# Optimization experiments

Measured on AMD Instinct MI355X. Metric: run time of the kernel, lower is better.

## Reference

```python
import jax, jax.numpy as jnp
import numpy as np

LN_EPS = 1e-5
NEG_SLOPE = 0.01  # torch LeakyReLU default


def layernorm(x, w, b):
    m = jnp.mean(x, axis=-1, keepdims=True)
    v = jnp.mean((x - m) ** 2, axis=-1, keepdims=True)
    return (x - m) * jax.lax.rsqrt(v + LN_EPS) * w + b


def setup_inputs() -> dict:
    key = jax.random.key(0)
    ks = jax.random.split(key, 12)
    B, T, C, E = 16, 1024, 768, 2
    d = C
    s = 0.02
    inp = {
        "x": jax.random.normal(ks[0], (B, T, C), jnp.float32),
        "ln1_w": jnp.ones((C,), jnp.float32),
        "ln1_b": jnp.zeros((C,), jnp.float32),
        "wqkv": jax.random.normal(ks[1], (C, 3 * C), jnp.float32) * s,
        "bqkv": jnp.zeros((3 * C,), jnp.float32),
        "wproj": jax.random.normal(ks[2], (C, C), jnp.float32) * s,
        "bproj": jnp.zeros((C,), jnp.float32),
        "ln2_w": jnp.ones((C,), jnp.float32),
        "ln2_b": jnp.zeros((C,), jnp.float32),
        "wg": jax.random.normal(ks[3], (C, E), jnp.float32) * s,
        # Experts module uses torch.randn (std 1); we scale down for numerics
        "w1": jax.random.normal(ks[4], (E, d, 4 * d), jnp.float32) * s,
        "w2": jax.random.normal(ks[5], (E, 4 * d, 4 * d), jnp.float32) * s,
        "w3": jax.random.normal(ks[6], (E, 4 * d, d), jnp.float32) * s,
        "n_head": 12,
    }
    return inp


def block_forward(x, ln1_w, ln1_b, wqkv, bqkv, wproj, bproj,
                  ln2_w, ln2_b, wg, w1, w2, w3, n_head):
    B, T, C = x.shape
    H = n_head
    hd = C // H
    E = wg.shape[-1]

    # ---- causal self-attention + residual ----
    h = layernorm(x, ln1_w, ln1_b)
    qkv = h @ wqkv + bqkv                      # [B,T,3C]
    q, k, v = jnp.split(qkv, 3, axis=-1)
    q = q.reshape(B, T, H, hd).transpose(0, 2, 1, 3)  # bhtd
    k = k.reshape(B, T, H, hd).transpose(0, 2, 1, 3)
    v = v.reshape(B, T, H, hd).transpose(0, 2, 1, 3)
    scores = jnp.einsum('bhqd,bhkd->bhqk', q, k) / jnp.sqrt(jnp.float32(hd))
    causal = jnp.tril(jnp.ones((T, T), bool))
    scores = jnp.where(causal, scores, jnp.finfo(scores.dtype).min)
    attn = jax.nn.softmax(scores, axis=-1)
    y = jnp.einsum('bhqk,bhkd->bhqd', attn, v)
    y = y.transpose(0, 2, 1, 3).reshape(B, T, C)
    x = x + (y @ wproj + bproj)

    # ---- MoE (top-2 gating, capacity dispatch) + residual ----
    h2 = layernorm(x, ln2_w, ln2_b)
    capacity = (T * 2) // E                    # capacity_factor = 1.0, top-2
    raw_gates = jax.nn.softmax(h2 @ wg, axis=-1)   # [B,T,E]

    idx1 = jnp.argmax(raw_gates, axis=-1)
    mask1 = jax.nn.one_hot(idx1, E, dtype=raw_gates.dtype)
    gate1 = jnp.sum(raw_gates * mask1, axis=-1)    # [B,T]
    gates2 = raw_gates * (1.0 - mask1)
    idx2 = jnp.argmax(gates2, axis=-1)
    mask2 = jax.nn.one_hot(idx2, E, dtype=raw_gates.dtype)
    gate2 = jnp.sum(raw_gates * mask2, axis=-1)
    denom = gate1 + gate2 + 1e-9
    gate1, gate2 = gate1 / denom, gate2 / denom

    # aux load-balancing loss (before capacity truncation)
    density = jnp.mean(mask1, axis=1)              # [B,E]
    density_proxy = jnp.mean(raw_gates, axis=1)    # [B,E]
    aux_loss = jnp.mean(density * density_proxy) * (E * E)

    # positions within each expert buffer (exclusive cumsum over tokens)
    pos1 = jnp.cumsum(mask1, axis=1) - mask1       # [B,T,E]
    mask1 = mask1 * (pos1 < capacity)
    mask1_count = jnp.sum(mask1, axis=1, keepdims=True)
    pos2 = (jnp.cumsum(mask2, axis=1) - mask2) + mask1_count
    mask2 = mask2 * (pos2 < capacity)

    oh1 = jax.nn.one_hot(pos1.astype(jnp.int32), capacity, dtype=raw_gates.dtype)
    oh2 = jax.nn.one_hot(pos2.astype(jnp.int32), capacity, dtype=raw_gates.dtype)
    combine = (gate1[..., None] * mask1)[..., None] * oh1 \
            + (gate2[..., None] * mask2)[..., None] * oh2   # [B,T,E,C]
    dispatch = (combine > 0).astype(h2.dtype)

    # dispatch -> per-expert batches
    expert_in = jnp.einsum('bnd,bnec->ebcd', h2, dispatch)   # [E,B,Cap,d]
    Bc = B * capacity
    ei = expert_in.reshape(E, Bc, C)
    lrelu = lambda z: jnp.where(z >= 0, z, NEG_SLOPE * z)
    hh = lrelu(jnp.einsum('end,edh->enh', ei, w1))
    hh = lrelu(jnp.einsum('end,edh->enh', hh, w2))
    eo = jnp.einsum('end,edh->enh', hh, w3).reshape(E, B, capacity, C)
    moe_out = jnp.einsum('ebcd,bnec->bnd', eo, combine)

    x = x + moe_out
    return x, aux_loss


def reference(x, ln1_w, ln1_b, wqkv, bqkv, wproj, bproj,
              ln2_w, ln2_b, wg, w1, w2, w3, n_head):
    return block_forward(x, ln1_w, ln1_b, wqkv, bqkv, wproj, bproj,
                         ln2_w, ln2_b, wg, w1, w2, w3, n_head)
```

## Files before the change

### kernel.cpp

```cpp
#include <hip/hip_runtime.h>
#include <cstdint>
#include <cstddef>

constexpr int B_  = 16;
constexpr int T_  = 1024;
constexpr int C_  = 768;
constexpr int H_  = 12;
constexpr int HD_ = 64;
constexpr int BT_ = B_ * T_;
constexpr int C3_ = 3 * C_;
constexpr int QK2_ = 2 * C_;
constexpr int FF_ = 4 * C_;
constexpr int MCH_ = 8192;

typedef __bf16 bf16x8 __attribute__((ext_vector_type(8)));
typedef float  floatx4 __attribute__((ext_vector_type(4)));
typedef unsigned short u16x8 __attribute__((ext_vector_type(8)));

__device__ inline float bf2f(unsigned short u) {
  union { unsigned int i; float f; } x; x.i = ((unsigned int)u) << 16; return x.f;
}
__device__ inline unsigned short f2bf(float f) {
  union { float f; unsigned int i; } x; x.f = f;
  unsigned int u = x.i;
  u += 0x7fffu + ((u >> 16) & 1u);
  return (unsigned short)(u >> 16);
}

#define GLOAD_LDS16(gp, lp)                                              \
  __builtin_amdgcn_global_load_lds(                                      \
      (__attribute__((address_space(1))) void*)(gp),                     \
      (__attribute__((address_space(3))) void*)(lp), 16, 0, 0)

__launch_bounds__(256)
__global__ void ln_kernel(const float* __restrict__ x, const float* __restrict__ w,
                          const float* __restrict__ b, unsigned short* __restrict__ out) {
  int row = blockIdx.x;
  int tid = threadIdx.x;
  const float* xr = x + (size_t)row * C_;
  float v0 = xr[tid], v1 = xr[tid + 256], v2 = xr[tid + 512];
  float s  = v0 + v1 + v2;
  float ss = v0 * v0 + v1 * v1 + v2 * v2;
#pragma unroll
  for (int off = 32; off > 0; off >>= 1) {
    s  += __shfl_down(s, off, 64);
    ss += __shfl_down(ss, off, 64);
  }
  __shared__ float red[8];
  int wid = tid >> 6;
  if ((tid & 63) == 0) { red[wid] = s; red[4 + wid] = ss; }
  __syncthreads();
  float st  = red[0] + red[1] + red[2] + red[3];
  float sst = red[4] + red[5] + red[6] + red[7];
  float mean = st * (1.0f / C_);
  float var  = sst * (1.0f / C_) - mean * mean;
  float rstd = rsqrtf(var + 1e-5f);
  unsigned short* orow = out + (size_t)row * C_;
  orow[tid]       = f2bf((v0 - mean) * rstd * w[tid]       + b[tid]);
  orow[tid + 256] = f2bf((v1 - mean) * rstd * w[tid + 256] + b[tid + 256]);
  orow[tid + 512] = f2bf((v2 - mean) * rstd * w[tid + 512] + b[tid + 512]);
}

__launch_bounds__(256)
__global__ void convT(const float* __restrict__ in, unsigned short* __restrict__ out,
                      int K, int N) {
  __shared__ float t[32][33];
  int n0 = blockIdx.x * 32, k0 = blockIdx.y * 32;
  int tx = threadIdx.x & 31, ty = threadIdx.x >> 5;
#pragma unroll
  for (int r = 0; r < 32; r += 8)
    t[r + ty][tx] = in[(size_t)(k0 + r + ty) * N + n0 + tx];
  __syncthreads();
#pragma unroll
  for (int r = 0; r < 32; r += 8)
    out[(size_t)(n0 + r + ty) * K + k0 + tx] = f2bf(t[tx][r + ty]);
}

template <int ACT, bool BIAS, bool RES, bool COMBINE, bool OUTBF16, bool VSPLIT = false>
__launch_bounds__(256)
__global__ void gemm_bf16(const unsigned short* __restrict__ A,
                          const unsigned short* __restrict__ Bt,
                          const float* __restrict__ bias,
                          const float* __restrict__ Rres,
                          const float* __restrict__ gates2, int eidx,
                          void* __restrict__ Cout,
                          unsigned short* __restrict__ vtout,
                          int M, int N, int K) {
  __shared__ __attribute__((aligned(16))) unsigned short Als[8192];
  __shared__ __attribute__((aligned(16))) unsigned short Bls[8192];
  const int tid  = threadIdx.x;
  const int wave = tid >> 6, lane = tid & 63;
  const int wr = wave >> 1, wc = wave & 1;
  const int m0 = blockIdx.y * 128, n0 = blockIdx.x * 128;

  const int srow = wave * 32 + (lane >> 3);
  const int skg  = (lane & 7) ^ ((lane >> 3) & 7);
  const unsigned short* Ap = A  + (size_t)(m0 + srow) * K + skg * 8;
  const unsigned short* Bp = Bt + (size_t)(n0 + srow) * K + skg * 8;
  unsigned short* AlsW = Als + wave * 2048;
  unsigned short* BlsW = Bls + wave * 2048;

  floatx4 acc[4][4];
#pragma unroll
  for (int i = 0; i < 4; ++i)
#pragma unroll
    for (int j = 0; j < 4; ++j) acc[i][j] = floatx4{0.f, 0.f, 0.f, 0.f};

  const int q  = lane >> 4;
  const int ml = lane & 15;
  const int rsw = ml & 7;

  for (int k0 = 0; k0 < K; k0 += 64) {
    __syncthreads();
#pragma unroll
    for (int i = 0; i < 4; ++i) {
      GLOAD_LDS16(Ap + (size_t)(i * 8) * K + k0, AlsW + i * 512);
      GLOAD_LDS16(Bp + (size_t)(i * 8) * K + k0, BlsW + i * 512);
    }
    __syncthreads();
#pragma unroll
    for (int ks = 0; ks < 2; ++ks) {
      const int p = (ks * 4 + q) ^ rsw;
      bf16x8 af[4], bfg[4];
#pragma unroll
      for (int i = 0; i < 4; ++i) {
        int ar = wr * 64 + i * 16 + ml;
        af[i]  = *(const bf16x8*)&Als[(ar * 8 + p) * 8];
        int br = wc * 64 + i * 16 + ml;
        bfg[i] = *(const bf16x8*)&Bls[(br * 8 + p) * 8];
      }
#pragma unroll
      for (int i = 0; i < 4; ++i)
#pragma unroll
        for (int j = 0; j < 4; ++j)
          acc[i][j] = __builtin_amdgcn_mfma_f32_16x16x32_bf16(af[i], bfg[j], acc[i][j], 0, 0, 0);
    }
  }

  const int rbase = q * 4;
#pragma unroll
  for (int i = 0; i < 4; ++i) {
    int row = m0 + wr * 64 + i * 16 + rbase;
#pragma unroll
    for (int j = 0; j < 4; ++j) {
      int col = n0 + wc * 64 + j * 16 + ml;
      float bcol = BIAS ? bias[col] : 0.f;
#pragma unroll
      for (int r = 0; r < 4; ++r) {
        float v = acc[i][j][r];
        if (BIAS) v += bcol;
        if (ACT == 1) v = (v >= 0.f) ? v : 0.01f * v;
        if (RES) v += Rres[(size_t)(row + r) * N + col];
        if (COMBINE) {
          float g = gates2[2 * (row + r) + eidx];
          float* op = (float*)Cout + (size_t)(row + r) * N + col;
          *op += g * v;
        } else if (VSPLIT) {
          if (col < QK2_) {
            ((unsigned short*)Cout)[(size_t)(row + r) * QK2_ + col] = f2bf(v);
          } else {
            vtout[(size_t)(col - QK2_) * BT_ + row + r] = f2bf(v);
          }
        } else if (OUTBF16) {
          ((unsigned short*)Cout)[(size_t)(row + r) * N + col] = f2bf(v);
        } else {
          ((float*)Cout)[(size_t)(row + r) * N + col] = v;
        }
      }
    }
  }
}

#define GB256_BAR()   asm volatile("s_barrier" ::: "memory")
#define GB256_LGKM0() asm volatile("s_waitcnt lgkmcnt(0)" ::: "memory")

template <int ACT, bool BIAS>
__launch_bounds__(512, 2)
__global__ void gemm256(const unsigned short* __restrict__ A,
                        const unsigned short* __restrict__ Bt,
                        const float* __restrict__ bias,
                        unsigned short* __restrict__ Cout,
                        int M, int N, int K) {
  __shared__ __attribute__((aligned(16))) unsigned short L[65536];
  const int tid = threadIdx.x;
  const int w = tid >> 6, l = tid & 63;
  const int wr = w >> 2, wc = w & 3;
  const int ml = l & 15, q = l >> 4;
  const int m0 = blockIdx.y * 256, n0 = blockIdx.x * 256;

  const int srow = l >> 2;
  const int sg   = ((l & 3) ^ ((l >> 3) & 3)) * 8;
  const unsigned short* Ast = A  + (size_t)(m0 + srow) * K + sg;
  const unsigned short* Bst = Bt + (size_t)(n0 + srow) * K + sg;
  const int ldsw = w * 1024;

#define STG(cb, mat, ks, srcp, kk)                                           \
  do {                                                                       \
    const unsigned short* _s = (srcp) + (size_t)(w * 32) * K + (kk) + (ks) * 32; \
    unsigned short* _d = L + (cb) * 32768 + (mat) * 16384 + (ks) * 8192 + ldsw;  \
    GLOAD_LDS16(_s, _d);                                                     \
    GLOAD_LDS16(_s + (size_t)16 * K, _d + 512);                              \
  } while (0)

  const int dphys = (q ^ ((ml >> 1) & 3)) * 8;
  const int aoff = (wr * 128 + ml) * 32 + dphys;
  const int boff = (wc * 64 + ml) * 32 + dphys;

  floatx4 acc[8][4];
#pragma unroll
  for (int m = 0; m < 8; ++m)
#pragma unroll
    for (int n = 0; n < 4; ++n) acc[m][n] = floatx4{0.f, 0.f, 0.f, 0.f};

  const int NT = K >> 6;

  STG(0, 0, 0, Ast, 0);  STG(0, 1, 0, Bst, 0);
  STG(0, 0, 1, Ast, 0);  STG(0, 1, 1, Bst, 0);
  STG(1, 0, 0, Ast, 64); STG(1, 1, 0, Bst, 64);
  asm volatile("s_waitcnt vmcnt(0)" ::: "memory");
  GB256_BAR();

  for (int j = 0; j < NT; ++j) {
    const int c = j & 1, nx = c ^ 1;
    const int kk1 = (j + 1) << 6, kk2 = (j + 2) << 6;
    const bool st1 = (j + 1 < NT), st2 = (j + 2 < NT);
    bf16x8 bA[4], bB[4];

#define LOAD_A(KS, MH)                                                       \
  _Pragma("unroll")                                                          \
  for (int mq = 0; mq < 4; ++mq)                                             \
    bA[mq] = *(const bf16x8*)&L[c * 32768 + (KS) * 8192 + aoff + ((MH) * 4 + mq) * 512];
#define LOAD_B(KS)                                                           \
  _Pragma("unroll")                                                          \
  for (int n = 0; n < 4; ++n)                                                \
    bB[n] = *(const bf16x8*)&L[c * 32768 + 16384 + (KS) * 8192 + boff + n * 512];
#define MFMA16(MH)                                                           \
  __builtin_amdgcn_s_setprio(1);                                             \
  _Pragma("unroll")                                                          \
  for (int mq = 0; mq < 4; ++mq)                                             \
    _Pragma("unroll")                                                        \
    for (int n = 0; n < 4; ++n)                                              \
      acc[(MH) * 4 + mq][n] = __builtin_amdgcn_mfma_f32_16x16x32_bf16(       \
          bA[mq], bB[n], acc[(MH) * 4 + mq][n], 0, 0, 0);                    \
  __builtin_amdgcn_s_setprio(0);

    LOAD_B(0); LOAD_A(0, 0);
    if (st1) STG(nx, 0, 1, Ast, kk1);
    GB256_BAR(); GB256_LGKM0();
    MFMA16(0);
    GB256_BAR();

    LOAD_A(0, 1);
    if (st1) STG(nx, 1, 1, Bst, kk1);
    GB256_BAR(); GB256_LGKM0();
    MFMA16(1);
    GB256_BAR();

    LOAD_B(1); LOAD_A(1, 0);
    if (st2) STG(c, 0, 0, Ast, kk2);
    GB256_BAR(); GB256_LGKM0();
    MFMA16(0);
    GB256_BAR();

    LOAD_A(1, 1);
    if (st2) STG(c, 1, 0, Bst, kk2);
    GB256_BAR(); GB256_LGKM0();
    MFMA16(1);
    if (st2)      asm volatile("s_waitcnt vmcnt(4)" ::: "memory");
    else if (st1) asm volatile("s_waitcnt vmcnt(0)" ::: "memory");
    GB256_BAR();
#undef LOAD_A
#undef LOAD_B
#undef MFMA16
  }

#pragma unroll
  for (int m = 0; m < 8; ++m) {
    const int row = m0 + wr * 128 + m * 16 + q * 4;
#pragma unroll
    for (int n = 0; n < 4; ++n) {
      const int col = n0 + wc * 64 + n * 16 + ml;
      const float bcol = BIAS ? bias[col] : 0.f;
#pragma unroll
      for (int r = 0; r < 4; ++r) {
        float v = acc[m][n][r];
        if (BIAS) v += bcol;
        if (ACT == 1) v = (v >= 0.f) ? v : 0.01f * v;
        Cout[(size_t)(row + r) * N + col] = f2bf(v);
      }
    }
  }
#undef STG
}

__launch_bounds__(256)
__global__ void attn_kernel(const unsigned short* __restrict__ qk,
                            const unsigned short* __restrict__ vT,
                            unsigned short* __restrict__ y) {
  __shared__ __attribute__((aligned(16))) unsigned short Qls[64 * 64];
  __shared__ __attribute__((aligned(16))) unsigned short K2[2][64 * 64];
  __shared__ __attribute__((aligned(16))) unsigned short V2[2][64 * 64];
  __shared__ __attribute__((aligned(16))) unsigned short Pls[4 * 16 * 72];

  const int tid  = threadIdx.x;
  const int wave = tid >> 6, lane = tid & 63;
  const int quad = lane >> 4, n = lane & 15;
  const int q0 = blockIdx.x * 64;
  const int bh = blockIdx.y;
  const int b = bh / H_, h = bh % H_;
  const size_t qbase = (size_t)b * T_ * QK2_ + (size_t)h * HD_;
  const size_t vbase = (size_t)h * HD_ * BT_ + (size_t)b * T_;

  const int r8 = lane >> 3;
  const int g  = (lane & 7) ^ r8;

#pragma unroll
  for (int i = 0; i < 2; ++i) {
    int row = wave * 16 + i * 8 + r8;
    GLOAD_LDS16(qk + qbase + (size_t)(q0 + row) * QK2_ + g * 8,
                Qls + wave * 1024 + i * 512);
  }

#define STAGE_KV(bf, k0)                                                      \
  do {                                                                        \
    _Pragma("unroll")                                                         \
    for (int i = 0; i < 2; ++i) {                                             \
      int row = wave * 16 + i * 8 + r8;                                       \
      GLOAD_LDS16(qk + qbase + (size_t)((k0) + row) * QK2_ + C_ + g * 8,      \
                  K2[bf] + wave * 1024 + i * 512);                            \
      GLOAD_LDS16(vT + vbase + (size_t)row * BT_ + (k0) + g * 8,              \
                  V2[bf] + wave * 1024 + i * 512);                            \
    }                                                                         \
  } while (0)

  STAGE_KV(0, 0);

  floatx4 O[4];
#pragma unroll
  for (int ct = 0; ct < 4; ++ct) O[ct] = floatx4{0.f, 0.f, 0.f, 0.f};
  float mrow[4] = {-1e30f, -1e30f, -1e30f, -1e30f};
  float lrow[4] = {0.f, 0.f, 0.f, 0.f};

  const int nkt = blockIdx.x + 1;
  unsigned short* Pw = Pls + wave * (16 * 72);

  for (int kt = 0; kt < nkt; ++kt) {
    const int cur = kt & 1;
    __syncthreads();
    if (kt + 1 < nkt) STAGE_KV(cur ^ 1, (kt + 1) << 6);

    floatx4 sacc[4];
#pragma unroll
    for (int ct = 0; ct < 4; ++ct) sacc[ct] = floatx4{0.f, 0.f, 0.f, 0.f};
#pragma unroll
    for (int ks = 0; ks < 2; ++ks) {
      const int ga = (ks * 4 + quad) ^ (n & 7);
      bf16x8 aq = *(const bf16x8*)&Qls[((wave * 16 + n) * 8 + ga) * 8];
#pragma unroll
      for (int ct = 0; ct < 4; ++ct) {
        bf16x8 kb = *(const bf16x8*)&K2[cur][((ct * 16 + n) * 8 + ga) * 8];
        sacc[ct] = __builtin_amdgcn_mfma_f32_16x16x32_bf16(aq, kb, sacc[ct], 0, 0, 0);
      }
    }

    float p[4][4];
#pragma unroll
    for (int ct = 0; ct < 4; ++ct)
#pragma unroll
      for (int r = 0; r < 4; ++r) p[ct][r] = sacc[ct][r] * 0.125f;
    if (kt == nkt - 1) {
      const int kgb = (kt << 6) + n, qgb = q0 + wave * 16 + quad * 4;
#pragma unroll
      for (int ct = 0; ct < 4; ++ct)
#pragma unroll
        for (int r = 0; r < 4; ++r)
          if (kgb + ct * 16 > qgb + r) p[ct][r] = -1e30f;
    }
#pragma unroll
    for (int r = 0; r < 4; ++r) {
      float tm = fmaxf(fmaxf(p[0][r], p[1][r]), fmaxf(p[2][r], p[3][r]));
      tm = fmaxf(tm, __shfl_xor(tm, 1, 64));
      tm = fmaxf(tm, __shfl_xor(tm, 2, 64));
      tm = fmaxf(tm, __shfl_xor(tm, 4, 64));
      tm = fmaxf(tm, __shfl_xor(tm, 8, 64));
      float mn = fmaxf(mrow[r], tm);
      float alpha = __expf(mrow[r] - mn);
      mrow[r] = mn;
      float ps = 0.f;
#pragma unroll
      for (int ct = 0; ct < 4; ++ct) {
        float pe = __expf(p[ct][r] - mn);
        p[ct][r] = pe;
        ps += pe;
      }
      ps += __shfl_xor(ps, 1, 64);
      ps += __shfl_xor(ps, 2, 64);
      ps += __shfl_xor(ps, 4, 64);
      ps += __shfl_xor(ps, 8, 64);
      lrow[r] = lrow[r] * alpha + ps;
      O[0][r] *= alpha; O[1][r] *= alpha; O[2][r] *= alpha; O[3][r] *= alpha;
    }

#pragma unroll
    for (int ct = 0; ct < 4; ++ct)
#pragma unroll
      for (int r = 0; r < 4; ++r)
        Pw[(quad * 4 + r) * 72 + ct * 16 + n] = f2bf(p[ct][r]);

#pragma unroll
    for (int ks = 0; ks < 2; ++ks) {
      bf16x8 pa = *(const bf16x8*)&Pw[n * 72 + (ks * 4 + quad) * 8];
      const int gv = (ks * 4 + quad) ^ (n & 7);
#pragma unroll
      for (int ct = 0; ct < 4; ++ct) {
        bf16x8 vb = *(const bf16x8*)&V2[cur][((ct * 16 + n) * 8 + gv) * 8];
        O[ct] = __builtin_amdgcn_mfma_f32_16x16x32_bf16(pa, vb, O[ct], 0, 0, 0);
      }
    }
  }

#pragma unroll
  for (int r = 0; r < 4; ++r) {
    float inv = 1.0f / lrow[r];
    int row = q0 + wave * 16 + quad * 4 + r;
    unsigned short* dst = y + ((size_t)b * T_ + row) * C_ + h * HD_;
#pragma unroll
    for (int ct = 0; ct < 4; ++ct)
      dst[ct * 16 + n] = f2bf(O[ct][r] * inv);
  }
#undef STAGE_KV
}

__launch_bounds__(256)
__global__ void gate_kernel(const unsigned short* __restrict__ h2,
                            const float* __restrict__ wg,
                            float* __restrict__ gates) {
  int wave = threadIdx.x >> 6, lane = threadIdx.x & 63;
  int t = blockIdx.x * 4 + wave;
  const unsigned short* hr = h2 + (size_t)t * C_;
  float a0 = 0.0f, a1 = 0.0f;
#pragma unroll
  for (int i = 0; i < 12; ++i) {
    int d = lane + 64 * i;
    float hv = bf2f(hr[d]);
    a0 += hv * wg[2 * d];
    a1 += hv * wg[2 * d + 1];
  }
#pragma unroll
  for (int off = 32; off > 0; off >>= 1) {
    a0 += __shfl_down(a0, off, 64);
    a1 += __shfl_down(a1, off, 64);
  }
  if (lane == 0) {
    float m  = fmaxf(a0, a1);
    float e0 = __expf(a0 - m), e1 = __expf(a1 - m);
    float invs = 1.0f / (e0 + e1);
    float p0 = e0 * invs, p1 = e1 * invs;
    const float gnorm = 1.0f / (1.0f + 1e-9f);
    gates[2 * t]     = p0 * gnorm;
    gates[2 * t + 1] = p1 * gnorm;
  }
}

__launch_bounds__(1024)
__global__ void moe_stats_kernel(const float* __restrict__ gates,
                                 float* __restrict__ out_aux) {
  int wave = threadIdx.x >> 6, lane = threadIdx.x & 63;
  float c0 = 0.f, sp0 = 0.f, sp1 = 0.f;
#pragma unroll
  for (int j = 0; j < 16; ++j) {
    int t = wave * T_ + lane + 64 * j;
    float p0 = gates[2 * t], p1 = gates[2 * t + 1];
    c0  += (p1 > p0) ? 0.f : 1.f;
    sp0 += p0;
    sp1 += p1;
  }
#pragma unroll
  for (int off = 32; off > 0; off >>= 1) {
    c0  += __shfl_down(c0, off, 64);
    sp0 += __shfl_down(sp0, off, 64);
    sp1 += __shfl_down(sp1, off, 64);
  }
  __shared__ float red[16][3];
  if (lane == 0) { red[wave][0] = c0; red[wave][1] = sp0; red[wave][2] = sp1; }
  __syncthreads();
  if (threadIdx.x == 0) {
    float s = 0.f;
    for (int b = 0; b < B_; ++b) {
      float cc0 = red[b][0];
      float d0 = cc0 * (1.f / T_), d1 = (T_ - cc0) * (1.f / T_);
      float px0 = red[b][1] * (1.f / T_), px1 = red[b][2] * (1.f / T_);
      s += d0 * px0 + d1 * px1;
    }
    out_aux[0] = s * (4.f / 32.f);
  }
}

extern "C" void kernel_launch(void* const* d_in, const int* in_sizes, int n_in,
                              void* d_out, int out_size, void* d_ws, size_t ws_size,
                              hipStream_t stream) {
  const float* x     = (const float*)d_in[0];
  const float* ln1_w = (const float*)d_in[1];
  const float* ln1_b = (const float*)d_in[2];
  const float* wqkv  = (const float*)d_in[3];
  const float* bqkv  = (const float*)d_in[4];
  const float* wproj = (const float*)d_in[5];
  const float* bproj = (const float*)d_in[6];
  const float* ln2_w = (const float*)d_in[7];
  const float* ln2_b = (const float*)d_in[8];
  const float* wg    = (const float*)d_in[9];
  const float* w1    = (const float*)d_in[10];
  const float* w2    = (const float*)d_in[11];
  const float* w3    = (const float*)d_in[12];
  float* out = (float*)d_out;

  unsigned short* wsu   = (unsigned short*)d_ws;
  unsigned short* wqkvT = wsu;
  unsigned short* wprojT= wqkvT + (size_t)C3_ * C_;
  unsigned short* w1T   = wprojT + (size_t)C_ * C_;
  unsigned short* w2T   = w1T + (size_t)2 * FF_ * C_;
  unsigned short* w3T   = w2T + (size_t)2 * FF_ * FF_;
  unsigned short* hb    = w3T + (size_t)2 * C_ * FF_;
  unsigned short* region= hb + (size_t)BT_ * C_;
  unsigned short* qkb   = region;
  unsigned short* vTb   = region + (size_t)BT_ * QK2_;
  unsigned short* yb    = region + (size_t)BT_ * 3 * C_;
  unsigned short* hh1   = region;
  unsigned short* hh2   = region + (size_t)MCH_ * FF_;
  float* gates = (float*)(region + (size_t)BT_ * 4 * C_);

  convT<<<dim3(C3_ / 32, C_ / 32), 256, 0, stream>>>(wqkv, wqkvT, C_, C3_);
  convT<<<dim3(C_ / 32, C_ / 32), 256, 0, stream>>>(wproj, wprojT, C_, C_);
  for (int e = 0; e < 2; ++e) {
    convT<<<dim3(FF_ / 32, C_ / 32), 256, 0, stream>>>(
        w1 + (size_t)e * C_ * FF_, w1T + (size_t)e * FF_ * C_, C_, FF_);
    convT<<<dim3(FF_ / 32, FF_ / 32), 256, 0, stream>>>(
        w2 + (size_t)e * FF_ * FF_, w2T + (size_t)e * FF_ * FF_, FF_, FF_);
    convT<<<dim3(C_ / 32, FF_ / 32), 256, 0, stream>>>(
        w3 + (size_t)e * FF_ * C_, w3T + (size_t)e * C_ * FF_, FF_, C_);
  }

  ln_kernel<<<BT_, 256, 0, stream>>>(x, ln1_w, ln1_b, hb);
  gemm_bf16<0, true, false, false, true, true><<<dim3(C3_ / 128, BT_ / 128), 256, 0, stream>>>(
      hb, wqkvT, bqkv, nullptr, nullptr, 0, qkb, vTb, BT_, C3_, C_);
  attn_kernel<<<dim3(T_ / 64, B_ * H_), 256, 0, stream>>>(qkb, vTb, yb);
  gemm_bf16<0, true, true, false, false><<<dim3(C_ / 128, BT_ / 128), 256, 0, stream>>>(
      yb, wprojT, bproj, x, nullptr, 0, out, nullptr, BT_, C_, C_);

  ln_kernel<<<BT_, 256, 0, stream>>>(out, ln2_w, ln2_b, hb);
  gate_kernel<<<BT_ / 4, 256, 0, stream>>>(hb, wg, gates);
  moe_stats_kernel<<<1, 1024, 0, stream>>>(gates, out + (size_t)BT_ * C_);

  for (int e = 0; e < 2; ++e) {
    for (int c = 0; c < BT_ / MCH_; ++c) {
      const unsigned short* a = hb + (size_t)c * MCH_ * C_;
      gemm_bf16<1, false, false, false, true><<<dim3(FF_ / 128, MCH_ / 128), 256, 0, stream>>>(
          a, w1T + (size_t)e * FF_ * C_, nullptr, nullptr, nullptr, 0, hh1, nullptr, MCH_, FF_, C_);
      gemm256<1, false><<<dim3(FF_ / 256, MCH_ / 256), 512, 0, stream>>>(
          hh1, w2T + (size_t)e * FF_ * FF_, nullptr, hh2, MCH_, FF_, FF_);
      gemm_bf16<0, false, false, true, false><<<dim3(C_ / 128, MCH_ / 128), 256, 0, stream>>>(
          hh2, w3T + (size_t)e * C_ * FF_, nullptr, nullptr,
          gates + (size_t)2 * c * MCH_, e, out + (size_t)c * MCH_ * C_, nullptr, MCH_, C_, FF_);
    }
  }
}
```

Measured before the change: 1.811 ms.

## Double-buffer LDS fragment registers in gemm256 and use it for FFN1

```diff
diff --git a/kernel.cpp b/kernel.cpp
--- a/kernel.cpp
+++ b/kernel.cpp
@@ -171,8 +171,8 @@
   }
 }
 
-#define GB256_BAR()   asm volatile("s_barrier" ::: "memory")
-#define GB256_LGKM0() asm volatile("s_waitcnt lgkmcnt(0)" ::: "memory")
+#define GB256_BAR()  asm volatile("s_barrier" ::: "memory")
+#define SCHEDB0()    __builtin_amdgcn_sched_barrier(0)
 
 template <int ACT, bool BIAS>
 __launch_bounds__(512, 2)
@@ -220,59 +220,73 @@
   asm volatile("s_waitcnt vmcnt(0)" ::: "memory");
   GB256_BAR();
 
-  for (int j = 0; j < NT; ++j) {
-    const int c = j & 1, nx = c ^ 1;
-    const int kk1 = (j + 1) << 6, kk2 = (j + 2) << 6;
-    const bool st1 = (j + 1 < NT), st2 = (j + 2 < NT);
-    bf16x8 bA[4], bB[4];
-
-#define LOAD_A(KS, MH)                                                       \
+  bf16x8 rA0[4], rA1[4], rB0[4], rB1[4];
+#pragma unroll
+  for (int mq = 0; mq < 4; ++mq)
+    rA0[mq] = *(const bf16x8*)&L[aoff + mq * 512];
+#pragma unroll
+  for (int n = 0; n < 4; ++n)
+    rB0[n] = *(const bf16x8*)&L[16384 + boff + n * 512];
+
+#define LDA(dst, CB, KS, MH)                                                 \
   _Pragma("unroll")                                                          \
   for (int mq = 0; mq < 4; ++mq)                                             \
-    bA[mq] = *(const bf16x8*)&L[c * 32768 + (KS) * 8192 + aoff + ((MH) * 4 + mq) * 512];
-#define LOAD_B(KS)                                                           \
+    dst[mq] = *(const bf16x8*)&L[(CB) * 32768 + (KS) * 8192 + aoff + ((MH) * 4 + mq) * 512];
+#define LDB(dst, CB, KS)                                                     \
   _Pragma("unroll")                                                          \
   for (int n = 0; n < 4; ++n)                                                \
-    bB[n] = *(const bf16x8*)&L[c * 32768 + 16384 + (KS) * 8192 + boff + n * 512];
-#define MFMA16(MH)                                                           \
+    dst[n] = *(const bf16x8*)&L[(CB) * 32768 + 16384 + (KS) * 8192 + boff + n * 512];
+#define MFMA16(MH, AR, BR)                                                   \
   __builtin_amdgcn_s_setprio(1);                                             \
   _Pragma("unroll")                                                          \
   for (int mq = 0; mq < 4; ++mq)                                             \
     _Pragma("unroll")                                                        \
     for (int n = 0; n < 4; ++n)                                              \
       acc[(MH) * 4 + mq][n] = __builtin_amdgcn_mfma_f32_16x16x32_bf16(       \
-          bA[mq], bB[n], acc[(MH) * 4 + mq][n], 0, 0, 0);                    \
+          AR[mq], BR[n], acc[(MH) * 4 + mq][n], 0, 0, 0);                    \
   __builtin_amdgcn_s_setprio(0);
 
-    LOAD_B(0); LOAD_A(0, 0);
+  for (int j = 0; j < NT; ++j) {
+    const int c = j & 1, nx = c ^ 1;
+    const int kk1 = (j + 1) << 6, kk2 = (j + 2) << 6;
+    const bool st1 = (j + 1 < NT), st2 = (j + 2 < NT);
+
+    LDA(rA1, c, 0, 1);
     if (st1) STG(nx, 0, 1, Ast, kk1);
-    GB256_BAR(); GB256_LGKM0();
-    MFMA16(0);
+    SCHEDB0();
+    MFMA16(0, rA0, rB0);
     GB256_BAR();
 
-    LOAD_A(0, 1);
+    LDB(rB1, c, 1);
+    LDA(rA0, c, 1, 0);
     if (st1) STG(nx, 1, 1, Bst, kk1);
-    GB256_BAR(); GB256_LGKM0();
-    MFMA16(1);
+    SCHEDB0();
+    MFMA16(1, rA1, rB0);
     GB256_BAR();
 
-    LOAD_B(1); LOAD_A(1, 0);
+    LDA(rA1, c, 1, 1);
     if (st2) STG(c, 0, 0, Ast, kk2);
-    GB256_BAR(); GB256_LGKM0();
-    MFMA16(0);
+    SCHEDB0();
+    MFMA16(0, rA0, rB1);
+    if (st2)      asm volatile("s_waitcnt vmcnt(6)" ::: "memory");
+    else if (st1) asm volatile("s_waitcnt vmcnt(4)" ::: "memory");
+    else          asm volatile("s_waitcnt vmcnt(0)" ::: "memory");
     GB256_BAR();
 
-    LOAD_A(1, 1);
+    if (st1) {
+      LDA(rA0, nx, 0, 0);
+      LDB(rB0, nx, 0);
+    }
     if (st2) STG(c, 1, 0, Bst, kk2);
-    GB256_BAR(); GB256_LGKM0();
-    MFMA16(1);
-    if (st2)      asm volatile("s_waitcnt vmcnt(4)" ::: "memory");
-    else if (st1) asm volatile("s_waitcnt vmcnt(0)" ::: "memory");
+    SCHEDB0();
+    MFMA16(1, rA1, rB1);
+    if (st2) asm volatile("s_waitcnt vmcnt(4)" ::: "memory");
+    else     asm volatile("s_waitcnt vmcnt(0)" ::: "memory");
     GB256_BAR();
-#undef LOAD_A
-#undef LOAD_B
+  }
+#undef LDA
+#undef LDB
 #undef MFMA16
-  }
 
 #pragma unroll
   for (int m = 0; m < 8; ++m) {
@@ -554,8 +568,8 @@
   for (int e = 0; e < 2; ++e) {
     for (int c = 0; c < BT_ / MCH_; ++c) {
       const unsigned short* a = hb + (size_t)c * MCH_ * C_;
-      gemm_bf16<1, false, false, false, true><<<dim3(FF_ / 128, MCH_ / 128), 256, 0, stream>>>(
-          a, w1T + (size_t)e * FF_ * C_, nullptr, nullptr, nullptr, 0, hh1, nullptr, MCH_, FF_, C_);
+      gemm256<1, false><<<dim3(FF_ / 256, MCH_ / 256), 512, 0, stream>>>(
+          a, w1T + (size_t)e * FF_ * C_, nullptr, hh1, MCH_, FF_, C_);
       gemm256<1, false><<<dim3(FF_ / 256, MCH_ / 256), 512, 0, stream>>>(
           hh1, w2T + (size_t)e * FF_ * FF_, nullptr, hh2, MCH_, FF_, FF_);
       gemm_bf16<0, false, false, true, false><<<dim3(C_ / 128, MCH_ / 128), 256, 0, stream>>>(
```

Measured after the change: 1.878 ms. +3.7%, slower.

## Batch both MoE experts into z-dimension grids and merge weight transposes

Applied to the files above, without the earlier changes.

```diff
diff --git a/kernel.cpp b/kernel.cpp
--- a/kernel.cpp
+++ b/kernel.cpp
@@ -61,12 +61,27 @@
   orow[tid + 512] = f2bf((v2 - mean) * rstd * w[tid + 512] + b[tid + 512]);
 }
 
+struct CtJobs {
+  const float* in[8];
+  unsigned short* out[8];
+  int K[8], N[8], tX[8];
+  int t0[9];
+};
+
 __launch_bounds__(256)
-__global__ void convT(const float* __restrict__ in, unsigned short* __restrict__ out,
-                      int K, int N) {
+__global__ void convT_batch(CtJobs J) {
   __shared__ float t[32][33];
-  int n0 = blockIdx.x * 32, k0 = blockIdx.y * 32;
-  int tx = threadIdx.x & 31, ty = threadIdx.x >> 5;
+  int bid = blockIdx.x;
+  int ji = 0;
+#pragma unroll
+  for (int i = 0; i < 7; ++i) ji += (bid >= J.t0[i + 1]) ? 1 : 0;
+  const float* in = J.in[ji];
+  unsigned short* out = J.out[ji];
+  const int K = J.K[ji], N = J.N[ji];
+  const int lt = bid - J.t0[ji];
+  const int bx = lt % J.tX[ji], by = lt / J.tX[ji];
+  const int n0 = bx * 32, k0 = by * 32;
+  const int tx = threadIdx.x & 31, ty = threadIdx.x >> 5;
 #pragma unroll
   for (int r = 0; r < 32; r += 8)
     t[r + ty][tx] = in[(size_t)(k0 + r + ty) * N + n0 + tx];
@@ -76,7 +91,8 @@
     out[(size_t)(n0 + r + ty) * K + k0 + tx] = f2bf(t[tx][r + ty]);
 }
 
-template <int ACT, bool BIAS, bool RES, bool COMBINE, bool OUTBF16, bool VSPLIT = false>
+template <int ACT, bool BIAS, bool RES, bool COMBINE, bool OUTBF16,
+          bool VSPLIT = false, bool ZB = false>
 __launch_bounds__(256)
 __global__ void gemm_bf16(const unsigned short* __restrict__ A,
                           const unsigned short* __restrict__ Bt,
@@ -85,13 +101,31 @@
                           const float* __restrict__ gates2, int eidx,
                           void* __restrict__ Cout,
                           unsigned short* __restrict__ vtout,
-                          int M, int N, int K) {
+                          int M, int N, int K,
+                          size_t zsA, size_t zsB) {
   __shared__ __attribute__((aligned(16))) unsigned short Als[8192];
   __shared__ __attribute__((aligned(16))) unsigned short Bls[8192];
   const int tid  = threadIdx.x;
   const int wave = tid >> 6, lane = tid & 63;
   const int wr = wave >> 1, wc = wave & 1;
-  const int m0 = blockIdx.y * 128, n0 = blockIdx.x * 128;
+
+  if (ZB) {
+    A  += (size_t)blockIdx.z * zsA;
+    Bt += (size_t)blockIdx.z * zsB;
+    eidx = (int)blockIdx.z;
+  }
+
+  int bx = blockIdx.x, by = blockIdx.y;
+  {
+    const int nbx = gridDim.x;
+    const int nwg = nbx * gridDim.y;
+    if ((nwg & 7) == 0) {
+      const int bid = by * nbx + bx;
+      const int swz = (bid & 7) * (nwg >> 3) + (bid >> 3);
+      by = swz / nbx; bx = swz - by * nbx;
+    }
+  }
+  const int m0 = by * 128, n0 = bx * 128;
 
   const int srow = wave * 32 + (lane >> 3);
   const int skg  = (lane & 7) ^ ((lane >> 3) & 7);
@@ -154,7 +188,8 @@
         if (COMBINE) {
           float g = gates2[2 * (row + r) + eidx];
           float* op = (float*)Cout + (size_t)(row + r) * N + col;
-          *op += g * v;
+          if (ZB) atomicAdd(op, g * v);
+          else    *op += g * v;
         } else if (VSPLIT) {
           if (col < QK2_) {
             ((unsigned short*)Cout)[(size_t)(row + r) * QK2_ + col] = f2bf(v);
@@ -180,13 +215,18 @@
                         const unsigned short* __restrict__ Bt,
                         const float* __restrict__ bias,
                         unsigned short* __restrict__ Cout,
-                        int M, int N, int K) {
+                        int M, int N, int K,
+                        size_t zsA, size_t zsB, size_t zsC) {
   __shared__ __attribute__((aligned(16))) unsigned short L[65536];
   const int tid = threadIdx.x;
   const int w = tid >> 6, l = tid & 63;
   const int wr = w >> 2, wc = w & 3;
   const int ml = l & 15, q = l >> 4;
   const int m0 = blockIdx.y * 256, n0 = blockIdx.x * 256;
+
+  A    += (size_t)blockIdx.z * zsA;
+  Bt   += (size_t)blockIdx.z * zsB;
+  Cout += (size_t)blockIdx.z * zsC;
 
   const int srow = l >> 2;
   const int sg   = ((l & 3) ^ ((l >> 3) & 3)) * 8;
@@ -525,42 +565,79 @@
   unsigned short* qkb   = region;
   unsigned short* vTb   = region + (size_t)BT_ * QK2_;
   unsigned short* yb    = region + (size_t)BT_ * 3 * C_;
-  unsigned short* hh1   = region;
-  unsigned short* hh2   = region + (size_t)MCH_ * FF_;
-  float* gates = (float*)(region + (size_t)BT_ * 4 * C_);
-
-  convT<<<dim3(C3_ / 32, C_ / 32), 256, 0, stream>>>(wqkv, wqkvT, C_, C3_);
-  convT<<<dim3(C_ / 32, C_ / 32), 256, 0, stream>>>(wproj, wprojT, C_, C_);
-  for (int e = 0; e < 2; ++e) {
-    convT<<<dim3(FF_ / 32, C_ / 32), 256, 0, stream>>>(
-        w1 + (size_t)e * C_ * FF_, w1T + (size_t)e * FF_ * C_, C_, FF_);
-    convT<<<dim3(FF_ / 32, FF_ / 32), 256, 0, stream>>>(
-        w2 + (size_t)e * FF_ * FF_, w2T + (size_t)e * FF_ * FF_, FF_, FF_);
-    convT<<<dim3(C_ / 32, FF_ / 32), 256, 0, stream>>>(
-        w3 + (size_t)e * FF_ * C_, w3T + (size_t)e * C_ * FF_, FF_, C_);
+
+  const size_t regionElems = (size_t)BT_ * 4 * C_;
+  const size_t bigElems    = (size_t)4 * MCH_ * FF_;
+  const size_t baseElems   = (size_t)(region - wsu);
+  const bool   big = ws_size >= (baseElems + bigElems + 65536) * sizeof(unsigned short);
+
+  float* gates = (float*)(region + (big ? bigElems : regionElems));
+
+  {
+    CtJobs J;
+    int idx = 0, acc = 0;
+    auto add = [&](const float* in, unsigned short* outp, int K, int N) {
+      J.in[idx] = in; J.out[idx] = outp; J.K[idx] = K; J.N[idx] = N;
+      J.tX[idx] = N / 32; J.t0[idx] = acc;
+      acc += (N / 32) * (K / 32);
+      ++idx;
+    };
+    add(wqkv, wqkvT, C_, C3_);
+    add(wproj, wprojT, C_, C_);
+    for (int e = 0; e < 2; ++e) {
+      add(w1 + (size_t)e * C_ * FF_, w1T + (size_t)e * FF_ * C_, C_, FF_);
+      add(w2 + (size_t)e * FF_ * FF_, w2T + (size_t)e * FF_ * FF_, FF_, FF_);
+      add(w3 + (size_t)e * FF_ * C_, w3T + (size_t)e * C_ * FF_, FF_, C_);
+    }
+    J.t0[8] = acc;
+    convT_batch<<<acc, 256, 0, stream>>>(J);
   }
 
   ln_kernel<<<BT_, 256, 0, stream>>>(x, ln1_w, ln1_b, hb);
   gemm_bf16<0, true, false, false, true, true><<<dim3(C3_ / 128, BT_ / 128), 256, 0, stream>>>(
-      hb, wqkvT, bqkv, nullptr, nullptr, 0, qkb, vTb, BT_, C3_, C_);
+      hb, wqkvT, bqkv, nullptr, nullptr, 0, qkb, vTb, BT_, C3_, C_, 0, 0);
   attn_kernel<<<dim3(T_ / 64, B_ * H_), 256, 0, stream>>>(qkb, vTb, yb);
   gemm_bf16<0, true, true, false, false><<<dim3(C_ / 128, BT_ / 128), 256, 0, stream>>>(
-      yb, wprojT, bproj, x, nullptr, 0, out, nullptr, BT_, C_, C_);
+      yb, wprojT, bproj, x, nullptr, 0, out, nullptr, BT_, C_, C_, 0, 0);
 
   ln_kernel<<<BT_, 256, 0, stream>>>(out, ln2_w, ln2_b, hb);
   gate_kernel<<<BT_ / 4, 256, 0, stream>>>(hb, wg, gates);
   moe_stats_kernel<<<1, 1024, 0, stream>>>(gates, out + (size_t)BT_ * C_);
 
-  for (int e = 0; e < 2; ++e) {
+  if (big) {
+    unsigned short* hh1b = region;
+    unsigned short* hh2b = region + (size_t)2 * MCH_ * FF_;
     for (int c = 0; c < BT_ / MCH_; ++c) {
       const unsigned short* a = hb + (size_t)c * MCH_ * C_;
-      gemm_bf16<1, false, false, false, true><<<dim3(FF_ / 128, MCH_ / 128), 256, 0, stream>>>(
-          a, w1T + (size_t)e * FF_ * C_, nullptr, nullptr, nullptr, 0, hh1, nullptr, MCH_, FF_, C_);
-      gemm256<1, false><<<dim3(FF_ / 256, MCH_ / 256), 512, 0, stream>>>(
-          hh1, w2T + (size_t)e * FF_ * FF_, nullptr, hh2, MCH_, FF_, FF_);
-      gemm_bf16<0, false, false, true, false><<<dim3(C_ / 128, MCH_ / 128), 256, 0, stream>>>(
-          hh2, w3T + (size_t)e * C_ * FF_, nullptr, nullptr,
-          gates + (size_t)2 * c * MCH_, e, out + (size_t)c * MCH_ * C_, nullptr, MCH_, C_, FF_);
-    }
-  }
-}
+      gemm256<1, false><<<dim3(FF_ / 256, MCH_ / 256, 2), 512, 0, stream>>>(
+          a, w1T, nullptr, hh1b, MCH_, FF_, C_,
+          0, (size_t)FF_ * C_, (size_t)MCH_ * FF_);
+      gemm256<1, false><<<dim3(FF_ / 256, MCH_ / 256, 2), 512, 0, stream>>>(
+          hh1b, w2T, nullptr, hh2b, MCH_, FF_, FF_,
+          (size_t)MCH_ * FF_, (size_t)FF_ * FF_, (size_t)MCH_ * FF_);
+      gemm_bf16<0, false, false, true, false, false, true>
+          <<<dim3(C_ / 128, MCH_ / 128, 2), 256, 0, stream>>>(
+          hh2b, w3T, nullptr, nullptr,
+          gates + (size_t)2 * c * MCH_, 0, out + (size_t)c * MCH_ * C_, nullptr,
+          MCH_, C_, FF_, (size_t)MCH_ * FF_, (size_t)C_ * FF_);
+    }
+  } else {
+    unsigned short* hh1 = region;
+    unsigned short* hh2 = region + (size_t)MCH_ * FF_;
+    for (int e = 0; e < 2; ++e) {
+      for (int c = 0; c < BT_ / MCH_; ++c) {
+        const unsigned short* a = hb + (size_t)c * MCH_ * C_;
+        gemm_bf16<1, false, false, false, true><<<dim3(FF_ / 128, MCH_ / 128), 256, 0, stream>>>(
+            a, w1T + (size_t)e * FF_ * C_, nullptr, nullptr, nullptr, 0, hh1, nullptr,
+            MCH_, FF_, C_, 0, 0);
+        gemm_bf16<1, false, false, false, true><<<dim3(FF_ / 128, MCH_ / 128), 256, 0, stream>>>(
+            hh1, w2T + (size_t)e * FF_ * FF_, nullptr, nullptr, nullptr, 0, hh2, nullptr,
+            MCH_, FF_, FF_, 0, 0);
+        gemm_bf16<0, false, false, true, false><<<dim3(C_ / 128, MCH_ / 128), 256, 0, stream>>>(
+            hh2, w3T + (size_t)e * C_ * FF_, nullptr, nullptr,
+            gates + (size_t)2 * c * MCH_, e, out + (size_t)c * MCH_ * C_, nullptr,
+            MCH_, C_, FF_, 0, 0);
+      }
+    }
+  }
+}
```

Result: faster. 1.624 ms (-10.3%).
